# Kernel tuning notes

Measured on AMD Instinct MI355X. Metric: run time of the kernel, lower is better.

The kernel has to match this reference:

```python
import jax, jax.numpy as jnp
import numpy as np

DIMS = 1024
STATE = 2 * DIMS
EPS = 1e-8


def _rmsnorm(v, scale):
    # norm = ||v||_2 * d^{-1/2}
    d = v.shape[-1]
    n = jnp.sqrt(jnp.sum(v * v, axis=-1, keepdims=True)) * (d ** -0.5)
    return scale * v / (n + EPS)


def setup_inputs() -> dict:
    key = jax.random.key(0)
    ks = jax.random.split(key, 5)
    x = jax.random.normal(ks[0], (4, 2048, DIMS), dtype=jnp.float32)
    ls_scale = jnp.ones((DIMS // 2,), dtype=jnp.float32)
    rs_scale = jnp.ones((DIMS // 2,), dtype=jnp.float32)
    split_scale = jnp.full((DIMS,), 0.1, dtype=jnp.float32)
    sk = (1.0 / DIMS) ** 0.5
    Wk = jax.random.uniform(ks[1], (DIMS, STATE), jnp.float32, -sk, sk)
    Wugg = jax.random.uniform(ks[2], (DIMS, 3 * STATE), jnp.float32, -sk, sk)
    so = (1.0 / STATE) ** 0.5
    Wout = jax.random.uniform(ks[3], (STATE, DIMS), jnp.float32, -so, so)
    return {"x": x, "ls_scale": ls_scale, "rs_scale": rs_scale,
            "split_scale": split_scale, "Wk": Wk, "Wugg": Wugg, "Wout": Wout}


def reference(x, ls_scale, rs_scale, split_scale, Wk, Wugg, Wout):
    residual = x
    # RMS_split norm (output_dim=None)
    xl, xr = jnp.split(x, 2, axis=-1)
    xn = jnp.concatenate([_rmsnorm(xl, ls_scale), _rmsnorm(xr, rs_scale)], axis=-1)
    xn = xn * split_scale

    K = jax.nn.sigmoid(xn @ Wk)                      # [B,S,STATE]
    u, g_in, g_out = jnp.split(xn @ Wugg, 3, axis=-1)
    u = u * jax.nn.sigmoid(g_in) * (1.0 - K)

    # linear recurrence: h_0 = u_0; h_t = K_{t-1} * h_{t-1} + u_t
    a = jnp.concatenate([jnp.ones_like(K[..., :1, :]), K[..., :-1, :]], axis=-2)

    def combine(lhs, rhs):
        aL, bL = lhs
        aR, bR = rhs
        return (aL * aR, bL * aR + bR)

    _, h = jax.lax.associative_scan(combine, (a, u), axis=1)
    outputs = h * jax.nn.sigmoid(g_out)
    y = outputs @ Wout
    return y + residual
```

## Files before the change

### kernel.cpp

```cpp
#include <hip/hip_runtime.h>
#include <hip/hip_bf16.h>
#include <hip/hip_fp8.h>
#include <stdint.h>

#define DIMS 1024
#define STATE 2048
#define BATCH 4
#define SEQ 2048
#define TOKENS 8192
#define N1 8192
#define NCHUNK 16
#define CHUNKL (SEQ / NCHUNK)

typedef __hip_bfloat16 bf16;
typedef unsigned char u8;
typedef unsigned short u16;
typedef __attribute__((ext_vector_type(4))) float f32x4;
typedef __attribute__((ext_vector_type(16))) float f32x16;
typedef __attribute__((ext_vector_type(2))) long v2i64;
typedef __attribute__((ext_vector_type(4))) int v4i;
typedef __attribute__((ext_vector_type(8))) int v8i;

#define XN_SCALE 32.0f
#define W1_SCALE 256.0f
#define H_SCALE  32.0f
#define W2_SCALE 256.0f
#define INV_SCALE (1.0f / 8192.0f)

__device__ __forceinline__ float sigmoidf_(float x) {
  return 1.0f / (1.0f + __expf(-x));
}

__device__ __forceinline__ u8 to_fp8(float f) {
  __hip_fp8_e4m3 h(f);
  return h.__x;
}

__device__ __forceinline__ float b2f(u16 v) {
  union { uint32_t u; float f; } w;
  w.u = ((uint32_t)v) << 16;
  return w.f;
}

__device__ __forceinline__ u16 f2b(float f) {
  bf16 h = __float2bfloat16(f);
  return *(u16*)&h;
}

__device__ __forceinline__ void async_copy16(const void* g, void* l) {
  __builtin_amdgcn_global_load_lds(
      (const __attribute__((address_space(1))) void*)(uintptr_t)g,
      (__attribute__((address_space(3))) void*)(uint32_t)(uintptr_t)l,
      16, 0, 0);
}

__device__ __forceinline__ int swz32(int row, int kc) {
  int line = row >> 1;
  int sub = ((row & 1) << 2) | kc;
  return (line << 3) | (sub ^ (line & 7));
}
__device__ __forceinline__ void swz32_dec(int c, int& row, int& kc) {
  int line = c >> 3;
  int sub = (c & 7) ^ (line & 7);
  row = (line << 1) | (sub >> 2);
  kc = sub & 3;
}

__device__ __forceinline__ int xcd_swz(int wg, int nwg) {
  return (wg & 7) * (nwg >> 3) + (wg >> 3);
}

__global__ __launch_bounds__(256) void transpose_fp8_kernel(
    const float* __restrict__ W, u8* __restrict__ Wt, int K, int N,
    int stream_base, int interleave, float scale) {
  __shared__ float tile[32][33];
  int tx = threadIdx.x & 31;
  int ty = threadIdx.x >> 5;
  long col = (long)blockIdx.x * 32 + tx;
  long rowb = (long)blockIdx.y * 32;
#pragma unroll
  for (int i = 0; i < 32; i += 8)
    tile[ty + i][tx] = W[(rowb + ty + i) * N + col];
  __syncthreads();
  long ocol = rowb + tx;
  long orow = (long)blockIdx.x * 32 + ty;
#pragma unroll
  for (int i = 0; i < 32; i += 8) {
    long n = orow + i;
    long dstrow = interleave ? (((n & 2047) << 2) | (stream_base + (n >> 11))) : n;
    Wt[dstrow * K + ocol] = to_fp8(tile[tx][ty + i] * scale);
  }
}

__global__ __launch_bounds__(256) void rmsnorm_kernel(
    const float* __restrict__ x, const float* __restrict__ ls,
    const float* __restrict__ rs, const float* __restrict__ ss,
    u8* __restrict__ xn8) {
  int token = blockIdx.x;
  int tid = threadIdx.x;
  const float4* xt = (const float4*)(x + (long)token * DIMS);
  float4 v = xt[tid];
  float s = v.x * v.x + v.y * v.y + v.z * v.z + v.w * v.w;
#pragma unroll
  for (int d = 32; d > 0; d >>= 1) s += __shfl_down(s, d);
  __shared__ float parts[4];
  if ((tid & 63) == 0) parts[tid >> 6] = s;
  __syncthreads();
  int j = tid * 4;
  bool left = j < 512;
  float sum = left ? (parts[0] + parts[1]) : (parts[2] + parts[3]);
  float n = sqrtf(sum * (1.0f / 512.0f));
  float inv = 1.0f / (n + 1e-8f);
  const float4* sc = (const float4*)(left ? ls : rs);
  float4 g = sc[left ? tid : tid - 128];
  float4 p = ((const float4*)ss)[tid];
  u8 q[4];
  q[0] = to_fp8(v.x * g.x * inv * p.x * XN_SCALE);
  q[1] = to_fp8(v.y * g.y * inv * p.y * XN_SCALE);
  q[2] = to_fp8(v.z * g.z * inv * p.z * XN_SCALE);
  q[3] = to_fp8(v.w * g.w * inv * p.w * XN_SCALE);
  *(uint32_t*)(xn8 + (long)token * DIMS + j) = *(uint32_t*)q;
}

__device__ __forceinline__ void g1f8_stage(const u8* __restrict__ A,
                                           const u8* __restrict__ Bt,
                                           long arow0, long brow0, int k0,
                                           int wave, int lane, u8* As, u8* Bs) {
  const int K = DIMS;
#pragma unroll
  for (int i = 0; i < 4; i++) {
    int c = (wave * 4 + i) * 64 + lane;
    int row, kc; swz32_dec(c, row, kc);
    async_copy16(A + (arow0 + row) * K + k0 + kc * 16, (char*)As + (wave * 4 + i) * 1024);
  }
#pragma unroll
  for (int i = 0; i < 2; i++) {
    int c = (wave * 2 + i) * 64 + lane;
    int row, kc; swz32_dec(c, row, kc);
    async_copy16(Bt + (brow0 + row) * K + k0 + kc * 16, (char*)Bs + (wave * 2 + i) * 1024);
  }
}

__device__ __forceinline__ v8i ld_frag64(const u8* base, int row, int q4) {
  v4i lo = *(const v4i*)(base + swz32(row, q4 * 2) * 16);
  v4i hi = *(const v4i*)(base + swz32(row, q4 * 2 + 1) * 16);
  return __builtin_shufflevector(lo, hi, 0, 1, 2, 3, 4, 5, 6, 7);
}

__global__ __launch_bounds__(256, 2) void gemm1_fp8(
    const u8* __restrict__ A, const u8* __restrict__ Bt,
    uint32_t* __restrict__ AU, u16* __restrict__ GO) {
  __shared__ __align__(16) u8 As0[256 * 64], As1[256 * 64];
  __shared__ __align__(16) u8 Bs0[128 * 64], Bs1[128 * 64];
  __shared__ __align__(16) u8 occ_pad[8192];
  int tid = threadIdx.x;
  int lane = tid & 63, wave = tid >> 6;
  int wm = wave & 1, wn = wave >> 1;
  int wg = xcd_swz(blockIdx.y * gridDim.x + blockIdx.x, gridDim.x * gridDim.y);
  int bx = wg & 63;
  int by = wg >> 6;
  long arow0 = (long)by * 256;
  long brow0 = (long)bx * 128;
  int m_lane = lane & 31, q4 = lane >> 5;
  if (tid == 0) occ_pad[0] = 0;
  f32x16 acc[4][2] = {};

  g1f8_stage(A, Bt, arow0, brow0, 0, wave, lane, As0, Bs0);
  __syncthreads();

  for (int it = 0; it < 16; ++it) {
    const u8* Asc = (it & 1) ? As1 : As0;
    const u8* Bsc = (it & 1) ? Bs1 : Bs0;
    u8* Asn = (it & 1) ? As0 : As1;
    u8* Bsn = (it & 1) ? Bs0 : Bs1;
    if (it + 1 < 16)
      g1f8_stage(A, Bt, arow0, brow0, (it + 1) * 64, wave, lane, Asn, Bsn);
    v8i af[4], bf[2];
#pragma unroll
    for (int mt = 0; mt < 4; mt++)
      af[mt] = ld_frag64(Asc, wm * 128 + mt * 32 + m_lane, q4);
#pragma unroll
    for (int nt = 0; nt < 2; nt++)
      bf[nt] = ld_frag64(Bsc, wn * 64 + nt * 32 + m_lane, q4);
#pragma unroll
    for (int mt = 0; mt < 4; mt++)
#pragma unroll
      for (int nt = 0; nt < 2; nt++)
        acc[mt][nt] = __builtin_amdgcn_mfma_scale_f32_32x32x64_f8f6f4(
            bf[nt], af[mt], acc[mt][nt], 0, 0, 0, 127,
            0, 127);
    __syncthreads();
  }

#pragma unroll
  for (int mt = 0; mt < 4; mt++) {
    long row = arow0 + wm * 128 + mt * 32 + m_lane;
    long rb = row * STATE;
#pragma unroll
    for (int nt = 0; nt < 2; nt++) {
#pragma unroll
      for (int g = 0; g < 4; g++) {
        long col = brow0 + wn * 64 + nt * 32 + g * 8 + q4 * 4;
        long ch = col >> 2;
        float kraw = acc[mt][nt][g * 4 + 0] * INV_SCALE;
        float uraw = acc[mt][nt][g * 4 + 1] * INV_SCALE;
        float gin  = acc[mt][nt][g * 4 + 2] * INV_SCALE;
        float gout = acc[mt][nt][g * 4 + 3] * INV_SCALE;
        float ah = sigmoidf_(kraw);
        float uu = uraw * sigmoidf_(gin) * (1.0f - ah);
        u16 pr[2];
        pr[0] = f2b(ah);
        pr[1] = f2b(uu);
        AU[rb + ch] = *(uint32_t*)pr;
        GO[rb + ch] = f2b(sigmoidf_(gout));
      }
    }
  }
}

__device__ __forceinline__ void g2f8_stage(const u8* __restrict__ A,
                                           const u8* __restrict__ Bt,
                                           long arow0, long brow0, int k0,
                                           int wave, int lane, u8* As, u8* Bs) {
  const int K = STATE;
#pragma unroll
  for (int i = 0; i < 4; i++) {
    int c = (wave * 4 + i) * 64 + lane;
    int vrow, kc; swz32_dec(c, vrow, kc);
    async_copy16(A + (arow0 + (vrow >> 1)) * K + k0 + (vrow & 1) * 64 + kc * 16,
                 (char*)As + (wave * 4 + i) * 1024);
  }
#pragma unroll
  for (int i = 0; i < 4; i++) {
    int c = (wave * 4 + i) * 64 + lane;
    int vrow, kc; swz32_dec(c, vrow, kc);
    async_copy16(Bt + (brow0 + (vrow >> 1)) * K + k0 + (vrow & 1) * 64 + kc * 16,
                 (char*)Bs + (wave * 4 + i) * 1024);
  }
}

__global__ __launch_bounds__(256, 2) void gemm2_fp8(
    const u8* __restrict__ A, const u8* __restrict__ Bt,
    float* __restrict__ C, const float* __restrict__ resid) {
  __shared__ __align__(16) u8 As0[128 * 128], As1[128 * 128];
  __shared__ __align__(16) u8 Bs0[128 * 128], Bs1[128 * 128];
  int tid = threadIdx.x;
  int lane = tid & 63, wave = tid >> 6;
  int wm = wave & 1, wn = wave >> 1;
  int wg = xcd_swz(blockIdx.y * gridDim.x + blockIdx.x, gridDim.x * gridDim.y);
  int bx = wg & (gridDim.x - 1);
  int by = wg >> 3;
  long arow0 = (long)by * 128;
  long brow0 = (long)bx * 128;
  int m_lane = lane & 31, q4 = lane >> 5;
  f32x16 acc[2][2] = {};

  g2f8_stage(A, Bt, arow0, brow0, 0, wave, lane, As0, Bs0);
  __syncthreads();

  for (int it = 0; it < 16; ++it) {
    const u8* Asc = (it & 1) ? As1 : As0;
    const u8* Bsc = (it & 1) ? Bs1 : Bs0;
    u8* Asn = (it & 1) ? As0 : As1;
    u8* Bsn = (it & 1) ? Bs0 : Bs1;
    if (it + 1 < 16)
      g2f8_stage(A, Bt, arow0, brow0, (it + 1) * 128, wave, lane, Asn, Bsn);
#pragma unroll
    for (int ks = 0; ks < 2; ks++) {
      v8i af[2], bf[2];
#pragma unroll
      for (int mt = 0; mt < 2; mt++)
        af[mt] = ld_frag64(Asc, (wm * 64 + mt * 32 + m_lane) * 2 + ks, q4);
#pragma unroll
      for (int nt = 0; nt < 2; nt++)
        bf[nt] = ld_frag64(Bsc, (wn * 64 + nt * 32 + m_lane) * 2 + ks, q4);
#pragma unroll
      for (int mt = 0; mt < 2; mt++)
#pragma unroll
        for (int nt = 0; nt < 2; nt++)
          acc[mt][nt] = __builtin_amdgcn_mfma_scale_f32_32x32x64_f8f6f4(
              bf[nt], af[mt], acc[mt][nt], 0, 0, 0, 127, 0, 127);
    }
    __syncthreads();
  }
#pragma unroll
  for (int mt = 0; mt < 2; mt++) {
    long row = arow0 + wm * 64 + mt * 32 + m_lane;
#pragma unroll
    for (int nt = 0; nt < 2; nt++) {
#pragma unroll
      for (int g = 0; g < 4; g++) {
        long col = brow0 + wn * 64 + nt * 32 + g * 8 + q4 * 4;
        float4 rv = *(const float4*)(resid + row * DIMS + col);
        float4 ov;
        ov.x = acc[mt][nt][g * 4 + 0] * INV_SCALE + rv.x;
        ov.y = acc[mt][nt][g * 4 + 1] * INV_SCALE + rv.y;
        ov.z = acc[mt][nt][g * 4 + 2] * INV_SCALE + rv.z;
        ov.w = acc[mt][nt][g * 4 + 3] * INV_SCALE + rv.w;
        *(float4*)(C + row * DIMS + col) = ov;
      }
    }
  }
}

__global__ __launch_bounds__(256) void chunk_summary_kernel(
    const uint32_t* __restrict__ AU, float* __restrict__ carryA,
    float* __restrict__ carryU) {
  int b = blockIdx.x;
  int ch = blockIdx.y * 256 + threadIdx.x;
  int chunk = blockIdx.z;
  int t0 = chunk * CHUNKL;
  const uint32_t* base = AU + (long)b * SEQ * STATE + ch;
  float ap = 1.0f;
  if (chunk != 0) ap = b2f((u16)(base[(long)(t0 - 1) * STATE] & 0xffff));
  float A = 1.0f, U = 0.0f;
#pragma unroll 8
  for (int t = t0; t < t0 + CHUNKL; t++) {
    uint32_t w = base[(long)t * STATE];
    float ah = b2f((u16)(w & 0xffff));
    float u  = b2f((u16)(w >> 16));
    A *= ap;
    U = ap * U + u;
    ap = ah;
  }
  int cidx = (b * NCHUNK + chunk) * STATE + ch;
  carryA[cidx] = A;
  carryU[cidx] = U;
}

__global__ __launch_bounds__(256) void carry_scan_kernel(
    const float* __restrict__ carryA, const float* __restrict__ carryU,
    float* __restrict__ carryIn) {
  int idx = blockIdx.x * 256 + threadIdx.x;
  int b = idx >> 11;
  int ch = idx & 2047;
  float h = 0.0f;
#pragma unroll
  for (int c = 0; c < NCHUNK; c++) {
    int cidx = (b * NCHUNK + c) * STATE + ch;
    carryIn[cidx] = h;
    h = carryA[cidx] * h + carryU[cidx];
  }
}

__global__ __launch_bounds__(256) void scan_chunk_kernel(
    const uint32_t* __restrict__ AU, const u16* __restrict__ GO,
    const float* __restrict__ carryIn, u8* __restrict__ sco8) {
  int b = blockIdx.x;
  int c0 = blockIdx.y * 32;
  int chunk = blockIdx.z;
  int tstart = chunk * CHUNKL;
  __shared__ float a_s[32][65], u_s[32][65], h_s[32][65];
  int tid = threadIdx.x;
  int lane = tid & 63, wave = tid >> 6;
  int cc = tid & 31;
  int tq = tid >> 5;

  float carryH[8], carryK[8];
#pragma unroll
  for (int i = 0; i < 8; i++) {
    int ch = c0 + wave * 8 + i;
    carryH[i] = carryIn[(b * NCHUNK + chunk) * STATE + ch];
    carryK[i] = (chunk == 0)
                    ? 1.0f
                    : b2f((u16)(AU[((long)(b * SEQ + tstart - 1)) * STATE + ch] & 0xffff));
  }

  float g_r[8];
  for (int t0 = tstart; t0 < tstart + CHUNKL; t0 += 64) {
#pragma unroll
    for (int i = 0; i < 8; i++) {
      int t = tq * 8 + i;
      long idx = ((long)(b * SEQ + t0 + t)) * STATE + c0 + cc;
      uint32_t w = AU[idx];
      a_s[cc][t] = b2f((u16)(w & 0xffff));
      u_s[cc][t] = b2f((u16)(w >> 16));
      g_r[i] = b2f(GO[idx]);
    }
    __syncthreads();
#pragma unroll
    for (int i = 0; i < 8; i++) {
      int ch = wave * 8 + i;
      float aK = a_s[ch][lane];
      float u = u_s[ch][lane];
      float a = __shfl_up(aK, 1);
      if (lane == 0) a = carryK[i];
      float A = a, U = u;
#pragma unroll
      for (int d = 1; d < 64; d <<= 1) {
        float Au = __shfl_up(A, d);
        float Uu = __shfl_up(U, d);
        if (lane >= d) { U += A * Uu; A *= Au; }
      }
      float h = U + A * carryH[i];
      carryH[i] = __shfl(h, 63);
      carryK[i] = __shfl(aK, 63);
      h_s[ch][lane] = h;
    }
    __syncthreads();
#pragma unroll
    for (int i = 0; i < 8; i++) {
      int t = tq * 8 + i;
      sco8[((long)(b * SEQ + t0 + t)) * STATE + c0 + cc] =
          to_fp8(h_s[cc][t] * g_r[i] * H_SCALE);
    }
    __syncthreads();
  }
}

extern "C" void kernel_launch(void* const* d_in, const int* in_sizes, int n_in,
                              void* d_out, int out_size, void* d_ws, size_t ws_size,
                              hipStream_t stream) {
  const float* x    = (const float*)d_in[0];
  const float* ls   = (const float*)d_in[1];
  const float* rs   = (const float*)d_in[2];
  const float* ss   = (const float*)d_in[3];
  const float* Wk   = (const float*)d_in[4];
  const float* Wugg = (const float*)d_in[5];
  const float* Wout = (const float*)d_in[6];
  float* out = (float*)d_out;

  char* ws = (char*)d_ws;
  u8*   W1f8 = (u8*)ws;
  u8*   W2f8 = (u8*)(ws + 8388608);
  u8*   xn8  = (u8*)(ws + 10485760);
  uint32_t* AU = (uint32_t*)(ws + 18874368);
  u16*  GOb  = (u16*)(ws + 18874368 + 67108864);
  u8*   sco8 = (u8*)(ws + 18874368 + 67108864 + 33554432);
  float* carryA  = (float*)xn8;
  float* carryU  = carryA + BATCH * NCHUNK * STATE;
  float* carryIn = carryU + BATCH * NCHUNK * STATE;

  transpose_fp8_kernel<<<dim3(STATE / 32, DIMS / 32), 256, 0, stream>>>(
      Wk, W1f8, DIMS, STATE, 0, 1, W1_SCALE);
  transpose_fp8_kernel<<<dim3(3 * STATE / 32, DIMS / 32), 256, 0, stream>>>(
      Wugg, W1f8, DIMS, 3 * STATE, 1, 1, W1_SCALE);
  transpose_fp8_kernel<<<dim3(DIMS / 32, STATE / 32), 256, 0, stream>>>(
      Wout, W2f8, STATE, DIMS, 0, 0, W2_SCALE);

  rmsnorm_kernel<<<TOKENS, 256, 0, stream>>>(x, ls, rs, ss, xn8);

  gemm1_fp8<<<dim3(N1 / 128, TOKENS / 256), 256, 0, stream>>>(xn8, W1f8, AU, GOb);

  chunk_summary_kernel<<<dim3(BATCH, STATE / 256, NCHUNK), 256, 0, stream>>>(
      AU, carryA, carryU);
  carry_scan_kernel<<<dim3(BATCH * STATE / 256), 256, 0, stream>>>(
      carryA, carryU, carryIn);
  scan_chunk_kernel<<<dim3(BATCH, STATE / 32, NCHUNK), 256, 0, stream>>>(
      AU, GOb, carryIn, sco8);

  gemm2_fp8<<<dim3(DIMS / 128, TOKENS / 128), 256, 0, stream>>>(
      sco8, W2f8, out, x);
}
```

Before: 379.1 us.

## Triple-buffer gemm1 K-loop with vmcnt waits and fold carry scan into chunk scan

The fp8 GEMM1 main loop moves from double to triple LDS buffering. It prefetches two stages ahead, and each iteration does a manual s_waitcnt vmcnt plus one barrier where there used to be two __syncthreads. MFMA issue priority is raised with s_setprio, and the occupancy padding array is removed, so LDS use now comes from the triple buffers. Separately, the carry_scan kernel launch is removed: each scan_chunk block now recomputes its incoming carry by serially combining the preceding chunk summaries. This saves a launch at the cost of redundant reads, which grow with chunk index.

```diff
diff --git a/kernel.cpp b/kernel.cpp
--- a/kernel.cpp
+++ b/kernel.cpp
@@ -122,6 +122,12 @@
   *(uint32_t*)(xn8 + (long)token * DIMS + j) = *(uint32_t*)q;
 }
 
+__device__ __forceinline__ v8i ld_frag64(const u8* base, int row, int q4) {
+  v4i lo = *(const v4i*)(base + swz32(row, q4 * 2) * 16);
+  v4i hi = *(const v4i*)(base + swz32(row, q4 * 2 + 1) * 16);
+  return __builtin_shufflevector(lo, hi, 0, 1, 2, 3, 4, 5, 6, 7);
+}
+
 __device__ __forceinline__ void g1f8_stage(const u8* __restrict__ A,
                                            const u8* __restrict__ Bt,
                                            long arow0, long brow0, int k0,
@@ -141,18 +147,11 @@
   }
 }
 
-__device__ __forceinline__ v8i ld_frag64(const u8* base, int row, int q4) {
-  v4i lo = *(const v4i*)(base + swz32(row, q4 * 2) * 16);
-  v4i hi = *(const v4i*)(base + swz32(row, q4 * 2 + 1) * 16);
-  return __builtin_shufflevector(lo, hi, 0, 1, 2, 3, 4, 5, 6, 7);
-}
-
 __global__ __launch_bounds__(256, 2) void gemm1_fp8(
     const u8* __restrict__ A, const u8* __restrict__ Bt,
     uint32_t* __restrict__ AU, u16* __restrict__ GO) {
-  __shared__ __align__(16) u8 As0[256 * 64], As1[256 * 64];
-  __shared__ __align__(16) u8 Bs0[128 * 64], Bs1[128 * 64];
-  __shared__ __align__(16) u8 occ_pad[8192];
+  __shared__ __align__(16) u8 As[3][256 * 64];
+  __shared__ __align__(16) u8 Bs[3][128 * 64];
   int tid = threadIdx.x;
   int lane = tid & 63, wave = tid >> 6;
   int wm = wave & 1, wn = wave >> 1;
@@ -162,19 +161,21 @@
   long arow0 = (long)by * 256;
   long brow0 = (long)bx * 128;
   int m_lane = lane & 31, q4 = lane >> 5;
-  if (tid == 0) occ_pad[0] = 0;
   f32x16 acc[4][2] = {};
 
-  g1f8_stage(A, Bt, arow0, brow0, 0, wave, lane, As0, Bs0);
-  __syncthreads();
-
+  g1f8_stage(A, Bt, arow0, brow0, 0, wave, lane, As[0], Bs[0]);
+  g1f8_stage(A, Bt, arow0, brow0, 64, wave, lane, As[1], Bs[1]);
+
+  int cur = 0, nxt = 2;
   for (int it = 0; it < 16; ++it) {
-    const u8* Asc = (it & 1) ? As1 : As0;
-    const u8* Bsc = (it & 1) ? Bs1 : Bs0;
-    u8* Asn = (it & 1) ? As0 : As1;
-    u8* Bsn = (it & 1) ? Bs0 : Bs1;
-    if (it + 1 < 16)
-      g1f8_stage(A, Bt, arow0, brow0, (it + 1) * 64, wave, lane, Asn, Bsn);
+    if (it == 15) asm volatile("s_waitcnt vmcnt(0)" ::: "memory");
+    else          asm volatile("s_waitcnt vmcnt(6)" ::: "memory");
+    __builtin_amdgcn_s_barrier();
+    __builtin_amdgcn_sched_barrier(0);
+    if (it + 2 < 16)
+      g1f8_stage(A, Bt, arow0, brow0, (it + 2) * 64, wave, lane, As[nxt], Bs[nxt]);
+    const u8* Asc = As[cur];
+    const u8* Bsc = Bs[cur];
     v8i af[4], bf[2];
 #pragma unroll
     for (int mt = 0; mt < 4; mt++)
@@ -182,6 +183,7 @@
 #pragma unroll
     for (int nt = 0; nt < 2; nt++)
       bf[nt] = ld_frag64(Bsc, wn * 64 + nt * 32 + m_lane, q4);
+    __builtin_amdgcn_s_setprio(1);
 #pragma unroll
     for (int mt = 0; mt < 4; mt++)
 #pragma unroll
@@ -189,7 +191,9 @@
         acc[mt][nt] = __builtin_amdgcn_mfma_scale_f32_32x32x64_f8f6f4(
             bf[nt], af[mt], acc[mt][nt], 0, 0, 0, 127,
             0, 127);
-    __syncthreads();
+    __builtin_amdgcn_s_setprio(0);
+    cur = cur == 2 ? 0 : cur + 1;
+    nxt = nxt == 2 ? 0 : nxt + 1;
   }
 
 #pragma unroll
@@ -328,24 +332,10 @@
   carryU[cidx] = U;
 }
 
-__global__ __launch_bounds__(256) void carry_scan_kernel(
-    const float* __restrict__ carryA, const float* __restrict__ carryU,
-    float* __restrict__ carryIn) {
-  int idx = blockIdx.x * 256 + threadIdx.x;
-  int b = idx >> 11;
-  int ch = idx & 2047;
-  float h = 0.0f;
-#pragma unroll
-  for (int c = 0; c < NCHUNK; c++) {
-    int cidx = (b * NCHUNK + c) * STATE + ch;
-    carryIn[cidx] = h;
-    h = carryA[cidx] * h + carryU[cidx];
-  }
-}
-
 __global__ __launch_bounds__(256) void scan_chunk_kernel(
     const uint32_t* __restrict__ AU, const u16* __restrict__ GO,
-    const float* __restrict__ carryIn, u8* __restrict__ sco8) {
+    const float* __restrict__ carryA, const float* __restrict__ carryU,
+    u8* __restrict__ sco8) {
   int b = blockIdx.x;
   int c0 = blockIdx.y * 32;
   int chunk = blockIdx.z;
@@ -360,7 +350,12 @@
 #pragma unroll
   for (int i = 0; i < 8; i++) {
     int ch = c0 + wave * 8 + i;
-    carryH[i] = carryIn[(b * NCHUNK + chunk) * STATE + ch];
+    float h = 0.0f;
+    for (int c = 0; c < chunk; c++) {
+      int cidx = (b * NCHUNK + c) * STATE + ch;
+      h = carryA[cidx] * h + carryU[cidx];
+    }
+    carryH[i] = h;
     carryK[i] = (chunk == 0)
                     ? 1.0f
                     : b2f((u16)(AU[((long)(b * SEQ + tstart - 1)) * STATE + ch] & 0xffff));
@@ -429,7 +424,6 @@
   u8*   sco8 = (u8*)(ws + 18874368 + 67108864 + 33554432);
   float* carryA  = (float*)xn8;
   float* carryU  = carryA + BATCH * NCHUNK * STATE;
-  float* carryIn = carryU + BATCH * NCHUNK * STATE;
 
   transpose_fp8_kernel<<<dim3(STATE / 32, DIMS / 32), 256, 0, stream>>>(
       Wk, W1f8, DIMS, STATE, 0, 1, W1_SCALE);
@@ -444,10 +438,8 @@
 
   chunk_summary_kernel<<<dim3(BATCH, STATE / 256, NCHUNK), 256, 0, stream>>>(
       AU, carryA, carryU);
-  carry_scan_kernel<<<dim3(BATCH * STATE / 256), 256, 0, stream>>>(
-      carryA, carryU, carryIn);
   scan_chunk_kernel<<<dim3(BATCH, STATE / 32, NCHUNK), 256, 0, stream>>>(
-      AU, GOb, carryIn, sco8);
+      AU, GOb, carryA, carryU, sco8);
 
   gemm2_fp8<<<dim3(DIMS / 128, TOKENS / 128), 256, 0, stream>>>(
       sco8, W2f8, out, x);
```

Result: slower. 410.7 us (+8.3%).
